# Optimization experiments

Measured on AMD Instinct MI355X. Metric: run time of the kernel, lower is better.

Reference implementation:

```python
import math
import jax, jax.numpy as jnp
import numpy as np

B, C, S, E = 4, 8, 512, 512
H = 8
HD = E // H
STRIDE = 4
LOCAL_WINDOW = 32


def _sparse_causal_mask(seq_len, stride, window):
    # allowed[i, j]: local causal window (i-window <= j <= i) OR strided (j % stride == 0 and j < i)
    i = jnp.arange(seq_len)[:, None]
    j = jnp.arange(seq_len)[None, :]
    local = (j <= i) & (j >= i - window)
    strided = (j % stride == 0) & (j < i)
    return local | strided  # already subset of causal (j <= i)


def setup_inputs() -> dict:
    key = jax.random.key(0)
    ks = jax.random.split(key, 11)
    xavier = lambda k, fan: jax.random.uniform(k, (E, E), jnp.float32, -1.0, 1.0) * math.sqrt(6.0 / (2 * E))
    return {
        "query": jax.random.normal(ks[0], (B, C, S, E), jnp.float32),
        "key": jax.random.normal(ks[1], (B, C, S, E), jnp.float32),
        "value": jax.random.normal(ks[2], (B, C, S, E), jnp.float32),
        "Wq": xavier(ks[3], E), "bq": jnp.zeros((E,), jnp.float32),
        "Wk": xavier(ks[4], E), "bk": jnp.zeros((E,), jnp.float32),
        "Wv": xavier(ks[5], E), "bv": jnp.zeros((E,), jnp.float32),
        "Wo": xavier(ks[6], E), "bo": jnp.zeros((E,), jnp.float32),
    }


def reference(query, key, value, Wq, bq, Wk, bk, Wv, bv, Wo, bo):
    b, c, s, e = query.shape
    # projections (nn.Linear: x @ W.T + b)
    q = (query @ Wq.T + bq).reshape(b, c, s, H, HD).transpose(0, 3, 1, 2, 4)  # [b,h,c,s,d]
    k = (key @ Wk.T + bk).reshape(b, c, s, H, HD).transpose(0, 3, 1, 2, 4)
    v = (value @ Wv.T + bv).reshape(b, c, s, H, HD).transpose(0, 3, 1, 2, 4)
    scores = jnp.einsum("bhcsd,bhctd->bhcst", q, k) / math.sqrt(HD)  # [b,h,c,s,s]
    allowed = _sparse_causal_mask(s, STRIDE, LOCAL_WINDOW)  # [s,s] bool
    scores = jnp.where(allowed[None, None, None], scores, -jnp.inf)
    attn = jax.nn.softmax(scores, axis=-1)
    context = jnp.einsum("bhcst,bhctd->bhcsd", attn, v)
    context = context.transpose(0, 2, 3, 1, 4).reshape(b, c, s, e)  # [b,c,s,e]
    output = context @ Wo.T + bo
    return output, attn
```

## Files before the change

kernel.cpp:

```cpp
#include <hip/hip_runtime.h>
#include <math.h>

#define Bb 4
#define Cc 8
#define Ss 512
#define Ee 512
#define Hh 8
#define HDd 64
#define LOCALW 32
#define NTOK (Bb*Cc*Ss)
#define RS 40

typedef __attribute__((ext_vector_type(8))) __bf16 bf16x8;
typedef __attribute__((ext_vector_type(4))) float floatx4;
typedef __attribute__((ext_vector_type(4))) unsigned short ushort4v;

__device__ __forceinline__ unsigned short f2bf(float f) {
  union { float f; unsigned int i; } x; x.f = f;
  unsigned int r = x.i + 0x7fffu + ((x.i >> 16) & 1u);
  return (unsigned short)(r >> 16);
}

__device__ __forceinline__ float sexp(float x) { return __expf(fmaxf(x, -80.0f)); }

__global__ __launch_bounds__(256) void cvt3_f32_bf16(
    const float4* __restrict__ s0, const float4* __restrict__ s1, const float4* __restrict__ s2,
    ushort4v* __restrict__ d0, ushort4v* __restrict__ d1, ushort4v* __restrict__ d2, int n4)
{
  const float4* src = (blockIdx.y == 0) ? s0 : (blockIdx.y == 1) ? s1 : s2;
  ushort4v*    dst  = (blockIdx.y == 0) ? d0 : (blockIdx.y == 1) ? d1 : d2;
  int idx = blockIdx.x * blockDim.x + threadIdx.x;
  int stride = gridDim.x * blockDim.x;
  for (int i = idx; i < n4; i += stride) {
    float4 v = src[i];
    ushort4v o;
    o[0] = f2bf(v.x); o[1] = f2bf(v.y); o[2] = f2bf(v.z); o[3] = f2bf(v.w);
    dst[i] = o;
  }
}

__global__ __launch_bounds__(256) void cvtW_f32_bf16(
    const float4* __restrict__ s0, const float4* __restrict__ s1,
    const float4* __restrict__ s2, const float4* __restrict__ s3,
    ushort4v* __restrict__ d0, ushort4v* __restrict__ d1,
    ushort4v* __restrict__ d2, ushort4v* __restrict__ d3, int n4)
{
  const float4* src = (blockIdx.y == 0) ? s0 : (blockIdx.y == 1) ? s1 : (blockIdx.y == 2) ? s2 : s3;
  ushort4v*    dst  = (blockIdx.y == 0) ? d0 : (blockIdx.y == 1) ? d1 : (blockIdx.y == 2) ? d2 : d3;
  int idx = blockIdx.x * blockDim.x + threadIdx.x;
  int stride = gridDim.x * blockDim.x;
  for (int i = idx; i < n4; i += stride) {
    float4 v = src[i];
    ushort4v o;
    o[0] = f2bf(v.x); o[1] = f2bf(v.y); o[2] = f2bf(v.z); o[3] = f2bf(v.w);
    dst[i] = o;
  }
}

template <bool F32OUT>
__global__ __launch_bounds__(256, 4) void gemm_nt_bias3(
    const unsigned short* __restrict__ X0, const unsigned short* __restrict__ X1,
    const unsigned short* __restrict__ X2,
    const unsigned short* __restrict__ W0, const unsigned short* __restrict__ W1,
    const unsigned short* __restrict__ W2,
    const float* __restrict__ bias0, const float* __restrict__ bias1,
    const float* __restrict__ bias2,
    void* __restrict__ out0, void* __restrict__ out1, void* __restrict__ out2)
{
  const int z = blockIdx.z;
  const unsigned short* X = (z == 0) ? X0 : (z == 1) ? X1 : X2;
  const unsigned short* W = (z == 0) ? W0 : (z == 1) ? W1 : W2;
  const float* bias        = (z == 0) ? bias0 : (z == 1) ? bias1 : bias2;
  void* outv               = (z == 0) ? out0 : (z == 1) ? out1 : out2;

  __shared__ unsigned short As[128 * 64];
  __shared__ unsigned short Bs[128 * 64];

  const int K = Ee, N = Ee;
  const int lane = threadIdx.x & 63;
  const int wave = threadIdx.x >> 6;
  const int r16  = lane & 15;
  const int oct  = lane >> 4;
  const int m_blk = blockIdx.y * 128;
  const int n_blk = blockIdx.x * 128;
  const int wm = (wave >> 1) * 64;
  const int wn = (wave & 1) * 64;

  const int row8  = lane >> 3;
  const int chSt  = lane & 7;
  const int chSrc = chSt ^ row8;

  floatx4 acc[4][4];
  #pragma unroll
  for (int a = 0; a < 4; ++a)
    #pragma unroll
    for (int b = 0; b < 4; ++b)
      acc[a][b] = (floatx4)(0.0f);

  for (int kb = 0; kb < K; kb += 64) {
    __syncthreads();
    #pragma unroll
    for (int t = 0; t < 4; ++t) {
      const int rbase = t * 32 + wave * 8;
      const int arow = m_blk + rbase + row8;
      const int brow = n_blk + rbase + row8;
      __builtin_amdgcn_global_load_lds(
          (const __attribute__((address_space(1))) unsigned int*)(X + (size_t)arow * K + kb + chSrc * 8),
          (__attribute__((address_space(3))) unsigned int*)(As + rbase * 64), 16, 0, 0);
      __builtin_amdgcn_global_load_lds(
          (const __attribute__((address_space(1))) unsigned int*)(W + (size_t)brow * K + kb + chSrc * 8),
          (__attribute__((address_space(3))) unsigned int*)(Bs + rbase * 64), 16, 0, 0);
    }
    __syncthreads();

    #pragma unroll
    for (int s = 0; s < 2; ++s) {
      bf16x8 af[4], bfq[4];
      #pragma unroll
      for (int mi = 0; mi < 4; ++mi) {
        const int row = wm + mi * 16 + r16;
        af[mi] = *(const bf16x8*)(As + row * 64 + ((s * 4 + oct) ^ (r16 & 7)) * 8);
      }
      #pragma unroll
      for (int ni = 0; ni < 4; ++ni) {
        const int row = wn + ni * 16 + r16;
        bfq[ni] = *(const bf16x8*)(Bs + row * 64 + ((s * 4 + oct) ^ (r16 & 7)) * 8);
      }
      #pragma unroll
      for (int mi = 0; mi < 4; ++mi)
        #pragma unroll
        for (int ni = 0; ni < 4; ++ni)
          acc[mi][ni] = __builtin_amdgcn_mfma_f32_16x16x32_bf16(af[mi], bfq[ni], acc[mi][ni], 0, 0, 0);
    }
  }

  #pragma unroll
  for (int mi = 0; mi < 4; ++mi)
    #pragma unroll
    for (int ni = 0; ni < 4; ++ni)
      #pragma unroll
      for (int r = 0; r < 4; ++r) {
        const int m = m_blk + wm + mi * 16 + oct * 4 + r;
        const int n = n_blk + wn + ni * 16 + r16;
        const float val = acc[mi][ni][r] + bias[n];
        if (F32OUT) ((float*)outv)[(size_t)m * N + n] = val;
        else        ((unsigned short*)outv)[(size_t)m * N + n] = f2bf(val);
      }
}

__global__ __launch_bounds__(512, 4) void attn_kernel(
    const unsigned short* __restrict__ Q,
    const unsigned short* __restrict__ Kb,
    const unsigned short* __restrict__ V,
    float* __restrict__ attn_out,
    unsigned short* __restrict__ ctx)
{
  __shared__ unsigned short VT[HDd][Ss];
  __shared__ unsigned short scr[8][16 * RS];

  const int slice = blockIdx.x;
  const int c  = slice & (Cc - 1);
  const int bh = slice >> 3;
  const int h  = bh & (Hh - 1);
  const int b  = bh >> 3;
  const size_t tokBase  = (size_t)(b * Cc + c) * Ss;
  const size_t attnBase = (size_t)slice * Ss * Ss;

  const int tid  = threadIdx.x;
  const int lane = tid & 63;
  const int wave = tid >> 6;
  const int r16  = lane & 15;
  const int oct  = lane >> 4;
  unsigned short* sw = scr[wave];

  {
    const int d0 = wave * 8;
    const unsigned short* vbase = V + tokBase * Ee + h * HDd + d0;
    #pragma unroll
    for (int pass = 0; pass < 4; ++pass) {
      const int j0 = pass * 128 + lane * 2;
      const uint4 ra = *(const uint4*)(vbase + (size_t)j0 * Ee);
      const uint4 rb = *(const uint4*)(vbase + (size_t)(j0 + 1) * Ee);
      const unsigned int aw[4] = {ra.x, ra.y, ra.z, ra.w};
      const unsigned int bw[4] = {rb.x, rb.y, rb.z, rb.w};
      #pragma unroll
      for (int k = 0; k < 8; ++k) {
        const unsigned int av = (k & 1) ? (aw[k >> 1] >> 16) : (aw[k >> 1] & 0xffffu);
        const unsigned int bv = (k & 1) ? (bw[k >> 1] >> 16) : (bw[k >> 1] & 0xffffu);
        *(unsigned int*)(&VT[d0 + k][j0 ^ (k << 3)]) = av | (bv << 16);
      }
    }
  }
  __syncthreads();

  const int rt0 = 2 * wave + blockIdx.y;
  for (int t = 0; t < 2; ++t) {
    const int rt = t ? (31 - rt0) : rt0;
    const int I  = rt * 16;
    const int i  = I + r16;

    const unsigned short* qrow = Q + (tokBase + i) * Ee + h * HDd + oct * 8;
    const bf16x8 qa0 = *(const bf16x8*)(qrow);
    const bf16x8 qa1 = *(const bf16x8*)(qrow + 32);
    const unsigned short* kbase = Kb + (tokBase + r16) * Ee + h * HDd + oct * 8;
    const int ij0 = i - 4 * oct;

    float m_a = -INFINITY, l_a = 0.0f, m_b = -INFINITY, l_b = 0.0f;
    const int farEnd = rt - 2;
    int ct = 0;
    for (; ct + 1 < farEnd; ct += 2) {
      const unsigned short* kr0 = kbase + (size_t)ct * (16 * Ee);
      const unsigned short* kr1 = kbase + (size_t)(ct + 1) * (16 * Ee);
      const bf16x8 ka0 = *(const bf16x8*)(kr0);
      const bf16x8 ka1 = *(const bf16x8*)(kr0 + 32);
      const bf16x8 kc0 = *(const bf16x8*)(kr1);
      const bf16x8 kc1 = *(const bf16x8*)(kr1 + 32);
      floatx4 a = (floatx4)(0.0f), a2 = (floatx4)(0.0f);
      a  = __builtin_amdgcn_mfma_f32_16x16x32_bf16(ka0, qa0, a, 0, 0, 0);
      a  = __builtin_amdgcn_mfma_f32_16x16x32_bf16(ka1, qa1, a, 0, 0, 0);
      a2 = __builtin_amdgcn_mfma_f32_16x16x32_bf16(kc0, qa0, a2, 0, 0, 0);
      a2 = __builtin_amdgcn_mfma_f32_16x16x32_bf16(kc1, qa1, a2, 0, 0, 0);
      const float v0 = a[0] * 0.125f;
      const float w0 = a2[0] * 0.125f;
      float mn = fmaxf(m_a, v0);
      l_a = l_a * sexp(m_a - mn) + sexp(v0 - mn);
      m_a = mn;
      mn = fmaxf(m_b, w0);
      l_b = l_b * sexp(m_b - mn) + sexp(w0 - mn);
      m_b = mn;
    }
    for (; ct < farEnd; ++ct) {
      const unsigned short* krow = kbase + (size_t)ct * (16 * Ee);
      const bf16x8 kb0 = *(const bf16x8*)(krow);
      const bf16x8 kb1 = *(const bf16x8*)(krow + 32);
      floatx4 a = (floatx4)(0.0f);
      a = __builtin_amdgcn_mfma_f32_16x16x32_bf16(kb0, qa0, a, 0, 0, 0);
      a = __builtin_amdgcn_mfma_f32_16x16x32_bf16(kb1, qa1, a, 0, 0, 0);
      const float v0 = a[0] * 0.125f;
      const float mn = fmaxf(m_a, v0);
      l_a = l_a * sexp(m_a - mn) + sexp(v0 - mn);
      m_a = mn;
    }
    for (ct = (farEnd > 0 ? farEnd : 0); ct <= rt; ++ct) {
      const unsigned short* krow = kbase + (size_t)ct * (16 * Ee);
      const bf16x8 kb0 = *(const bf16x8*)(krow);
      const bf16x8 kb1 = *(const bf16x8*)(krow + 32);
      floatx4 a = (floatx4)(0.0f);
      a = __builtin_amdgcn_mfma_f32_16x16x32_bf16(kb0, qa0, a, 0, 0, 0);
      a = __builtin_amdgcn_mfma_f32_16x16x32_bf16(kb1, qa1, a, 0, 0, 0);
      const int dib = ij0 - 16 * ct;
      const float v0 = (dib >= 0)                   ? a[0] * 0.125f : -INFINITY;
      const float v1 = ((unsigned)(dib - 1) <= 32u) ? a[1] * 0.125f : -INFINITY;
      const float v2 = ((unsigned)(dib - 2) <= 32u) ? a[2] * 0.125f : -INFINITY;
      const float v3 = ((unsigned)(dib - 3) <= 32u) ? a[3] * 0.125f : -INFINITY;
      const float mx4 = fmaxf(fmaxf(v0, v1), fmaxf(v2, v3));
      const float mn = fmaxf(m_a, mx4);
      l_a = l_a * sexp(m_a - mn)
          + sexp(v0 - mn) + sexp(v1 - mn) + sexp(v2 - mn) + sexp(v3 - mn);
      m_a = mn;
    }
    float m = fmaxf(m_a, m_b);
    float l = l_a * sexp(m_a - m) + l_b * sexp(m_b - m);
    #pragma unroll
    for (int msk = 16; msk <= 32; msk <<= 1) {
      const float mo = __shfl_xor(m, msk, 64);
      const float lo = __shfl_xor(l, msk, 64);
      const float mn = fmaxf(m, mo);
      l = l * sexp(m - mn) + lo * sexp(mo - mn);
      m = mn;
    }
    const float cc = -m - __logf(l);

    const int jcMax = rt >> 1;
    floatx4 cacc[4];
    #pragma unroll
    for (int dt = 0; dt < 4; ++dt) cacc[dt] = (floatx4)(0.0f);
    float* attnRow = attn_out + attnBase + (size_t)i * Ss + oct * 4;
    unsigned short* swrow = sw + r16 * RS;

    for (int jc = 0; jc <= jcMax; ++jc) {
      #pragma unroll
      for (int h2 = 0; h2 < 2; ++h2) {
        const int ctp = 2 * jc + h2;
        float p0 = 0.0f, p1 = 0.0f, p2 = 0.0f, p3 = 0.0f;
        if (ctp <= rt) {
          const unsigned short* krow = kbase + (size_t)ctp * (16 * Ee);
          const bf16x8 kb0 = *(const bf16x8*)(krow);
          const bf16x8 kb1 = *(const bf16x8*)(krow + 32);
          floatx4 a = (floatx4)(0.0f);
          a = __builtin_amdgcn_mfma_f32_16x16x32_bf16(kb0, qa0, a, 0, 0, 0);
          a = __builtin_amdgcn_mfma_f32_16x16x32_bf16(kb1, qa1, a, 0, 0, 0);
          if (ctp < farEnd) {
            p0 = __expf(a[0] * 0.125f + cc);
          } else {
            const int dib = ij0 - 16 * ctp;
            if (dib >= 0)                   p0 = __expf(a[0] * 0.125f + cc);
            if ((unsigned)(dib - 1) <= 32u) p1 = __expf(a[1] * 0.125f + cc);
            if ((unsigned)(dib - 2) <= 32u) p2 = __expf(a[2] * 0.125f + cc);
            if ((unsigned)(dib - 3) <= 32u) p3 = __expf(a[3] * 0.125f + cc);
          }
        }
        __builtin_nontemporal_store((floatx4){p0, p1, p2, p3},
                                    (floatx4*)(attnRow + (size_t)ctp * 16));
        const unsigned int plo = (unsigned int)f2bf(p0) | ((unsigned int)f2bf(p1) << 16);
        const unsigned int phi = (unsigned int)f2bf(p2) | ((unsigned int)f2bf(p3) << 16);
        *(uint2*)(swrow + h2 * 16 + oct * 4) = make_uint2(plo, phi);
      }
      const bf16x8 pa = *(const bf16x8*)(swrow + oct * 8);
      #pragma unroll
      for (int dt = 0; dt < 4; ++dt) {
        const int d = dt * 16 + r16;
        const bf16x8 vb = *(const bf16x8*)(&VT[d][(jc * 32 + oct * 8) ^ ((d & 7) << 3)]);
        cacc[dt] = __builtin_amdgcn_mfma_f32_16x16x32_bf16(vb, pa, cacc[dt], 0, 0, 0);
      }
    }
    const floatx4 z4 = (floatx4)(0.0f);
    for (int ctz = 2 * (jcMax + 1); ctz < 32; ++ctz)
      __builtin_nontemporal_store(z4, (floatx4*)(attnRow + (size_t)ctz * 16));
    #pragma unroll
    for (int dt = 0; dt < 4; ++dt) {
      const unsigned int lo = (unsigned int)f2bf(cacc[dt][0]) | ((unsigned int)f2bf(cacc[dt][1]) << 16);
      const unsigned int hi = (unsigned int)f2bf(cacc[dt][2]) | ((unsigned int)f2bf(cacc[dt][3]) << 16);
      *(uint2*)(ctx + (tokBase + i) * Ee + h * HDd + dt * 16 + oct * 4) = make_uint2(lo, hi);
    }
  }
}

extern "C" void kernel_launch(void* const* d_in, const int* in_sizes, int n_in,
                              void* d_out, int out_size, void* d_ws, size_t ws_size,
                              hipStream_t stream) {
  const float* query = (const float*)d_in[0];
  const float* key_  = (const float*)d_in[1];
  const float* value = (const float*)d_in[2];
  const float* Wq = (const float*)d_in[3];
  const float* bq = (const float*)d_in[4];
  const float* Wk = (const float*)d_in[5];
  const float* bk = (const float*)d_in[6];
  const float* Wv = (const float*)d_in[7];
  const float* bv = (const float*)d_in[8];
  const float* Wo = (const float*)d_in[9];
  const float* bo = (const float*)d_in[10];

  float* out  = (float*)d_out;
  float* attn = out + (size_t)Bb*Cc*Ss*Ee;

  unsigned short* ws = (unsigned short*)d_ws;
  unsigned short* qb  = ws;
  unsigned short* kb  = qb  + (size_t)NTOK * Ee;
  unsigned short* vb  = kb  + (size_t)NTOK * Ee;
  unsigned short* Qw  = vb  + (size_t)NTOK * Ee;
  unsigned short* Kw  = Qw  + (size_t)NTOK * Ee;
  unsigned short* Vw  = Kw  + (size_t)NTOK * Ee;
  unsigned short* Cw  = Vw  + (size_t)NTOK * Ee;
  unsigned short* Wqb = Cw  + (size_t)NTOK * Ee;
  unsigned short* Wkb = Wqb + (size_t)Ee * Ee;
  unsigned short* Wvb = Wkb + (size_t)Ee * Ee;
  unsigned short* Wob = Wvb + (size_t)Ee * Ee;

  const int n4big = NTOK * Ee / 4;
  const int n4w   = Ee * Ee / 4;
  cvt3_f32_bf16<<<dim3(1024, 3), 256, 0, stream>>>(
      (const float4*)query, (const float4*)key_, (const float4*)value,
      (ushort4v*)qb, (ushort4v*)kb, (ushort4v*)vb, n4big);
  cvtW_f32_bf16<<<dim3(128, 4), 256, 0, stream>>>(
      (const float4*)Wq, (const float4*)Wk, (const float4*)Wv, (const float4*)Wo,
      (ushort4v*)Wqb, (ushort4v*)Wkb, (ushort4v*)Wvb, (ushort4v*)Wob, n4w);

  dim3 blk(256);
  gemm_nt_bias3<false><<<dim3(Ee / 128, NTOK / 128, 3), blk, 0, stream>>>(
      qb, kb, vb, Wqb, Wkb, Wvb, bq, bk, bv, Qw, Kw, Vw);

  attn_kernel<<<dim3(Bb*Hh*Cc, 2), 512, 0, stream>>>(Qw, Kw, Vw, attn, Cw);

  gemm_nt_bias3<true><<<dim3(Ee / 128, NTOK / 128, 1), blk, 0, stream>>>(
      Cw, Cw, Cw, Wob, Wob, Wob, bo, bo, bo, out, out, out);
}
```

Before: 487.2 us.

## Double-buffer GEMM LDS tiles with prefetch and remap blocks for locality

The projection GEMM now keeps two LDS buffers per operand and issues the global-to-LDS loads for the next K tile before the MFMAs on the current one, so load latency can overlap compute. Block IDs are remapped so that consecutive blocks spread across the M dimension, which is intended to change L2/cache locality. Bias values are hoisted into registers, and the f32 output uses nontemporal stores. Doubling LDS use means the occupancy hint drops from 4 to 2 blocks per CU, which trades latency hiding between blocks for the pipelining within each block.

```diff
diff --git a/kernel.cpp b/kernel.cpp
--- a/kernel.cpp
+++ b/kernel.cpp
@@ -57,8 +57,10 @@
   }
 }
 
+#define NXB (Ee/128)
+#define NYB (NTOK/128)
 template <bool F32OUT>
-__global__ __launch_bounds__(256, 4) void gemm_nt_bias3(
+__global__ __launch_bounds__(256, 2) void gemm_nt_bias3(
     const unsigned short* __restrict__ X0, const unsigned short* __restrict__ X1,
     const unsigned short* __restrict__ X2,
     const unsigned short* __restrict__ W0, const unsigned short* __restrict__ W1,
@@ -73,22 +75,24 @@
   const float* bias        = (z == 0) ? bias0 : (z == 1) ? bias1 : bias2;
   void* outv               = (z == 0) ? out0 : (z == 1) ? out1 : out2;
 
-  __shared__ unsigned short As[128 * 64];
-  __shared__ unsigned short Bs[128 * 64];
+  __shared__ unsigned short As[2][128 * 64];
+  __shared__ unsigned short Bs[2][128 * 64];
+
+  const int id   = blockIdx.x + NXB * blockIdx.y;
+  const int orig = (id & 7) * (NXB * NYB / 8) + (id >> 3);
+  const int m_blk = (orig >> 2) * 128;
+  const int n_blk = (orig & (NXB - 1)) * 128;
 
   const int K = Ee, N = Ee;
   const int lane = threadIdx.x & 63;
   const int wave = threadIdx.x >> 6;
   const int r16  = lane & 15;
   const int oct  = lane >> 4;
-  const int m_blk = blockIdx.y * 128;
-  const int n_blk = blockIdx.x * 128;
   const int wm = (wave >> 1) * 64;
   const int wn = (wave & 1) * 64;
 
   const int row8  = lane >> 3;
-  const int chSt  = lane & 7;
-  const int chSrc = chSt ^ row8;
+  const int chSrc = (lane & 7) ^ row8;
 
   floatx4 acc[4][4];
   #pragma unroll
@@ -97,21 +101,34 @@
     for (int b = 0; b < 4; ++b)
       acc[a][b] = (floatx4)(0.0f);
 
-  for (int kb = 0; kb < K; kb += 64) {
-    __syncthreads();
-    #pragma unroll
-    for (int t = 0; t < 4; ++t) {
-      const int rbase = t * 32 + wave * 8;
-      const int arow = m_blk + rbase + row8;
-      const int brow = n_blk + rbase + row8;
-      __builtin_amdgcn_global_load_lds(
-          (const __attribute__((address_space(1))) unsigned int*)(X + (size_t)arow * K + kb + chSrc * 8),
-          (__attribute__((address_space(3))) unsigned int*)(As + rbase * 64), 16, 0, 0);
-      __builtin_amdgcn_global_load_lds(
-          (const __attribute__((address_space(1))) unsigned int*)(W + (size_t)brow * K + kb + chSrc * 8),
-          (__attribute__((address_space(3))) unsigned int*)(Bs + rbase * 64), 16, 0, 0);
-    }
-    __syncthreads();
+  #pragma unroll
+  for (int t = 0; t < 4; ++t) {
+    const int rbase = t * 32 + wave * 8;
+    __builtin_amdgcn_global_load_lds(
+        (const __attribute__((address_space(1))) unsigned int*)(X + (size_t)(m_blk + rbase + row8) * K + chSrc * 8),
+        (__attribute__((address_space(3))) unsigned int*)(As[0] + rbase * 64), 16, 0, 0);
+    __builtin_amdgcn_global_load_lds(
+        (const __attribute__((address_space(1))) unsigned int*)(W + (size_t)(n_blk + rbase + row8) * K + chSrc * 8),
+        (__attribute__((address_space(3))) unsigned int*)(Bs[0] + rbase * 64), 16, 0, 0);
+  }
+  __syncthreads();
+
+  #pragma unroll
+  for (int kt = 0; kt < 8; ++kt) {
+    const int cur = kt & 1;
+    if (kt < 7) {
+      const int kb = (kt + 1) * 64;
+      #pragma unroll
+      for (int t = 0; t < 4; ++t) {
+        const int rbase = t * 32 + wave * 8;
+        __builtin_amdgcn_global_load_lds(
+            (const __attribute__((address_space(1))) unsigned int*)(X + (size_t)(m_blk + rbase + row8) * K + kb + chSrc * 8),
+            (__attribute__((address_space(3))) unsigned int*)(As[cur ^ 1] + rbase * 64), 16, 0, 0);
+        __builtin_amdgcn_global_load_lds(
+            (const __attribute__((address_space(1))) unsigned int*)(W + (size_t)(n_blk + rbase + row8) * K + kb + chSrc * 8),
+            (__attribute__((address_space(3))) unsigned int*)(Bs[cur ^ 1] + rbase * 64), 16, 0, 0);
+      }
+    }
 
     #pragma unroll
     for (int s = 0; s < 2; ++s) {
@@ -119,12 +136,12 @@
       #pragma unroll
       for (int mi = 0; mi < 4; ++mi) {
         const int row = wm + mi * 16 + r16;
-        af[mi] = *(const bf16x8*)(As + row * 64 + ((s * 4 + oct) ^ (r16 & 7)) * 8);
+        af[mi] = *(const bf16x8*)(As[cur] + row * 64 + ((s * 4 + oct) ^ (r16 & 7)) * 8);
       }
       #pragma unroll
       for (int ni = 0; ni < 4; ++ni) {
         const int row = wn + ni * 16 + r16;
-        bfq[ni] = *(const bf16x8*)(Bs + row * 64 + ((s * 4 + oct) ^ (r16 & 7)) * 8);
+        bfq[ni] = *(const bf16x8*)(Bs[cur] + row * 64 + ((s * 4 + oct) ^ (r16 & 7)) * 8);
       }
       #pragma unroll
       for (int mi = 0; mi < 4; ++mi)
@@ -132,7 +149,12 @@
         for (int ni = 0; ni < 4; ++ni)
           acc[mi][ni] = __builtin_amdgcn_mfma_f32_16x16x32_bf16(af[mi], bfq[ni], acc[mi][ni], 0, 0, 0);
     }
-  }
+    __syncthreads();
+  }
+
+  float bv[4];
+  #pragma unroll
+  for (int ni = 0; ni < 4; ++ni) bv[ni] = bias[n_blk + wn + ni * 16 + r16];
 
   #pragma unroll
   for (int mi = 0; mi < 4; ++mi)
@@ -142,8 +164,8 @@
       for (int r = 0; r < 4; ++r) {
         const int m = m_blk + wm + mi * 16 + oct * 4 + r;
         const int n = n_blk + wn + ni * 16 + r16;
-        const float val = acc[mi][ni][r] + bias[n];
-        if (F32OUT) ((float*)outv)[(size_t)m * N + n] = val;
+        const float val = acc[mi][ni][r] + bv[ni];
+        if (F32OUT) __builtin_nontemporal_store(val, (float*)outv + (size_t)m * N + n);
         else        ((unsigned short*)outv)[(size_t)m * N + n] = f2bf(val);
       }
 }
@@ -367,11 +389,11 @@
       (ushort4v*)Wqb, (ushort4v*)Wkb, (ushort4v*)Wvb, (ushort4v*)Wob, n4w);
 
   dim3 blk(256);
-  gemm_nt_bias3<false><<<dim3(Ee / 128, NTOK / 128, 3), blk, 0, stream>>>(
+  gemm_nt_bias3<false><<<dim3(NXB, NYB, 3), blk, 0, stream>>>(
       qb, kb, vb, Wqb, Wkb, Wvb, bq, bk, bv, Qw, Kw, Vw);
 
   attn_kernel<<<dim3(Bb*Hh*Cc, 2), 512, 0, stream>>>(Qw, Kw, Vw, attn, Cw);
 
-  gemm_nt_bias3<true><<<dim3(Ee / 128, NTOK / 128, 1), blk, 0, stream>>>(
+  gemm_nt_bias3<true><<<dim3(NXB, NYB, 1), blk, 0, stream>>>(
       Cw, Cw, Cw, Wob, Wob, Wob, bo, bo, bo, out, out, out);
 }
```

Result: no change. 484.7 us, median of 2 (-0.5%).
